# Kernel optimization log

Hardware: AMD Instinct MI355X
Metric: run time of the kernel (lower is better)

Reference implementation:

```python
import jax, jax.numpy as jnp
from jax import lax
import numpy as np

B, H, W = 16, 512, 512
NBINS = 256
MARGIN_EYE = 12
BLUR_SIZE = 5
ALPHA_SKIN, ALPHA_EYE, ALPHA_LIP = 0.3, 0.8, 0.1


def de_norm(x):
    return jnp.clip((x + 1.0) * 0.5, 0.0, 1.0)


def renorm(x):
    return x * 2.0 - 1.0


def _match_channel(src, ref, w_s, w_r):
    # src/ref: (P,) pixel values in [0,255]; w_s/w_r: (P,) mask weights
    b_s = jnp.clip(src.astype(jnp.int32), 0, NBINS - 1)
    b_r = jnp.clip(ref.astype(jnp.int32), 0, NBINS - 1)
    h_s = jnp.zeros((NBINS,), src.dtype).at[b_s].add(w_s)   # masked histogram
    h_r = jnp.zeros((NBINS,), ref.dtype).at[b_r].add(w_r)
    cdf_s = jnp.cumsum(h_s) / jnp.maximum(jnp.sum(h_s), 1e-6)
    cdf_r = jnp.cumsum(h_r) / jnp.maximum(jnp.sum(h_r), 1e-6)
    # CDF-matching transfer table (equiv. of cal_trans in PSGAN/EleGANt)
    table = jnp.clip(jnp.searchsorted(cdf_r, cdf_s), 0, NBINS - 1).astype(src.dtype)
    return table[b_s]


def masked_his_match(image_s, image_r, mask_s, mask_r):
    # image: (3,H,W), mask: (1,H,W)
    s = de_norm(image_s) * 255.0 * mask_s
    r = de_norm(image_r) * 255.0 * mask_r
    w_s = mask_s.reshape(-1)
    w_r = mask_r.reshape(-1)
    matched = jax.vmap(_match_channel, in_axes=(0, 0, None, None))(
        s.reshape(3, -1), r.reshape(3, -1), w_s, w_r).reshape(s.shape)
    matched = jnp.where(mask_s > 0, matched, s)  # only masked pixels replaced
    return renorm(matched / 255.0)


def expand_area(mask, margin):
    # morphological dilation (max pool) of (1,H,W) mask
    k = 2 * margin + 1
    return lax.reduce_window(mask, 0.0, lax.max, (1, k, k), (1, 1, 1), 'SAME')


def mask_blur(mask, blur_size):
    # box blur; 'valid' mode: blurred support kept inside original mask
    k = blur_size
    s = lax.reduce_window(mask, 0.0, lax.add, (1, k, k), (1, 1, 1), 'SAME') / float(k * k)
    return s * mask


def generate_pgt(image_s, image_r, mask_s, mask_r, lms_s, lms_r):
    pgt = image_s
    # skin (channel 1)
    m = mask_s[1:2]
    pgt = (1.0 - m) * pgt + m * masked_his_match(image_s, image_r, m, mask_r[1:2])
    # neck (channel 4)
    m = mask_s[4:5]
    pgt = (1.0 - m) * pgt + m * masked_his_match(image_s, image_r, m, mask_r[4:5])
    # lip (channel 0)
    m = mask_s[0:1]
    pgt = (1.0 - m) * pgt + m * masked_his_match(image_s, image_r, m, mask_r[0:1])
    # eyes (channels 2,3), dilated and intersected with skin
    m_se = expand_area(jnp.sum(mask_s[2:4], axis=0, keepdims=True), MARGIN_EYE) * mask_s[1:2]
    m_re = expand_area(jnp.sum(mask_r[2:4], axis=0, keepdims=True), MARGIN_EYE) * mask_r[1:2]
    eye_match = masked_his_match(image_s, image_r, m_se, m_re)
    mb = mask_blur(m_se, BLUR_SIZE)
    pgt = (1.0 - mb) * pgt + mb * eye_match
    # fine_align (reconstructed, simplified: per-region alpha blend of reference,
    # landmark warp omitted -- helper source not provided)
    for m, a in ((mask_s[1:2], ALPHA_SKIN), (m_se, ALPHA_EYE), (mask_s[0:1], ALPHA_LIP)):
        pgt = (1.0 - a * m) * pgt + (a * m) * image_r
    return pgt


def setup_inputs() -> dict:
    key = jax.random.key(0)
    ks = jax.random.split(key, 6)
    sources = jax.random.uniform(ks[0], (B, 3, H, W), jnp.float32, -1.0, 1.0)
    targets = jax.random.uniform(ks[1], (B, 3, H, W), jnp.float32, -1.0, 1.0)
    mask_srcs = (jax.random.uniform(ks[2], (B, 5, H, W)) < 0.3).astype(jnp.float32)
    mask_tars = (jax.random.uniform(ks[3], (B, 5, H, W)) < 0.3).astype(jnp.float32)
    lms_srcs = jax.random.uniform(ks[4], (B, 68, 2), jnp.float32, 0.0, float(H))
    lms_tars = jax.random.uniform(ks[5], (B, 68, 2), jnp.float32, 0.0, float(H))
    return {"sources": sources, "targets": targets, "mask_srcs": mask_srcs,
            "mask_tars": mask_tars, "lms_srcs": lms_srcs, "lms_tars": lms_tars}


def reference(sources, targets, mask_srcs, mask_tars, lms_srcs, lms_tars):
    # vmap over batch replaces the per-sample Python loop of ComposePGT.forward
    return jax.vmap(generate_pgt)(sources, targets, mask_srcs, mask_tars, lms_srcs, lms_tars)
```

## Files before the change

kernel.cpp:

```cpp
#include <hip/hip_runtime.h>
#include <stdint.h>

#define BB 16
#define HH 512
#define WW 512
#define HW (HH*WW)
#define NB 256


__device__ __forceinline__ float denorm255(float x) {
    return fminf(fmaxf((x + 1.0f) * 0.5f, 0.0f), 1.0f) * 255.0f;
}
__device__ __forceinline__ float renorm_lut(int t) {
    return ((float)t / 255.0f) * 2.0f - 1.0f;
}
__device__ __forceinline__ uint32_t alignb(uint32_t hi, uint32_t lo, int r) {
    return (uint32_t)(((((uint64_t)hi) << 32) | lo) >> (8 * r));
}

__global__ void __launch_bounds__(256) prep_hor_kernel(
    const float* __restrict__ ms, const float* __restrict__ mr,
    uint32_t* __restrict__ C, uint32_t* __restrict__ eh)
{
    int blk  = blockIdx.x;
    int side = blk >> 10;
    int rem  = blk & 1023;
    int b    = rem >> 6;
    int rg   = rem & 63;
    int r    = threadIdx.x >> 5;
    int c    = threadIdx.x & 31;
    int y    = (rg << 3) + r;

    const float* base = (side ? mr : ms) + (size_t)b * 5 * HW + (size_t)y * WW;

    float4 v[5][4];
    #pragma unroll
    for (int p = 0; p < 5; p++) {
        const float4* pp = (const float4*)(base + (size_t)p * HW);
        #pragma unroll
        for (int q = 0; q < 4; q++) v[p][q] = pp[c + 32 * q];
    }

    __shared__ uint32_t sE[8][128];
    size_t plane = (size_t)(side * BB + b);
    uint32_t* Crow = C + plane * (HW / 4) + y * 128;
    #pragma unroll
    for (int q = 0; q < 4; q++) {
        uint32_t wc = 0;
        #pragma unroll
        for (int j = 0; j < 4; j++) {
            float a0 = (&v[0][q].x)[j];
            float a1 = (&v[1][q].x)[j];
            float a2 = (&v[2][q].x)[j];
            float a3 = (&v[3][q].x)[j];
            float a4 = (&v[4][q].x)[j];
            uint32_t e  = (uint32_t)(a2 + a3);
            uint32_t pb = (a0 > 0.f ? 4u : 0u) | (a1 > 0.f ? 8u : 0u)
                        | (a4 > 0.f ? 16u : 0u);
            wc |= (e | pb) << (8 * j);
        }
        Crow[c + 32 * q] = wc;
        sE[r][c + 32 * q] = wc & 0x03030303u;
    }
    __syncthreads();

    uint32_t* Erow = eh + plane * (HW / 4) + y * 128;
    #pragma unroll
    for (int q = 0; q < 4; q++) {
        int w = c + 32 * q;
        uint32_t arr[7];
        #pragma unroll
        for (int i = 0; i < 7; i++) {
            int idx = w - 3 + i;
            arr[i] = (idx >= 0 && idx < 128) ? sE[r][idx] : 0u;
        }
        uint32_t acc = arr[3];
        #pragma unroll
        for (int s = 1; s <= 12; s++) {
            int a = s >> 2, rr = s & 3;
            uint32_t vp, vm;
            if (rr == 0) {
                vp = arr[3 + a];
                vm = arr[3 - a];
            } else {
                vp = alignb(arr[3 + a + 1], arr[3 + a], rr);
                int am = (s + 3) >> 2;
                vm = alignb(arr[3 - am + 1], arr[3 - am], 4 - rr);
            }
            acc |= vp | vm;
        }
        Erow[w] = acc;
    }
}

__global__ void __launch_bounds__(256) ver_kernel(
    const uint32_t* __restrict__ eh, uint32_t* __restrict__ C)
{
    int t   = blockIdx.x * 256 + threadIdx.x;
    int sb  = t >> 12;
    int rem = t & 4095;
    int yg  = rem >> 5;
    int ck  = rem & 31;
    int y0  = yg << 2;
    const uint4* P = (const uint4*)(eh + (size_t)sb * (HW / 4));
    auto R = [&](int y) -> uint4 {
        uint4 z = {0, 0, 0, 0};
        if (y < 0 || y >= HH) return z;
        return P[y * 32 + ck];
    };
    uint4 core = {0, 0, 0, 0};
    #pragma unroll
    for (int yy = -9; yy <= 12; yy++) {
        uint4 r = R(y0 + yy);
        core.x |= r.x; core.y |= r.y; core.z |= r.z; core.w |= r.w;
    }
    uint4 b0 = R(y0 - 12), b1 = R(y0 - 11), b2 = R(y0 - 10);
    uint4 a0 = R(y0 + 13), a1 = R(y0 + 14), a2 = R(y0 + 15);

    uint4* C4 = (uint4*)(C + (size_t)sb * (HW / 4));
    #pragma unroll
    for (int i = 0; i < 4; i++) {
        uint4 v = core;
        if (i == 0) { v.x|=b0.x|b1.x|b2.x; v.y|=b0.y|b1.y|b2.y; v.z|=b0.z|b1.z|b2.z; v.w|=b0.w|b1.w|b2.w; }
        if (i == 1) { v.x|=b1.x|b2.x|a0.x; v.y|=b1.y|b2.y|a0.y; v.z|=b1.z|b2.z|a0.z; v.w|=b1.w|b2.w|a0.w; }
        if (i == 2) { v.x|=b2.x|a0.x|a1.x; v.y|=b2.y|a0.y|a1.y; v.z|=b2.z|a0.z|a1.z; v.w|=b2.w|a0.w|a1.w; }
        if (i == 3) { v.x|=a0.x|a1.x|a2.x; v.y|=a0.y|a1.y|a2.y; v.z|=a0.z|a1.z|a2.z; v.w|=a0.w|a1.w|a2.w; }
        int idx = (y0 + i) * 32 + ck;
        uint4 cw = C4[idx];
        #pragma unroll
        for (int q = 0; q < 4; q++) {
            uint32_t vv = (&v.x)[q];
            uint32_t cc = (&cw.x)[q];
            uint32_t t3 = vv & (vv >> 1) & 0x01010101u;
            vv -= t3;
            uint32_t m1b = (cc >> 3) & 0x01010101u;
            vv &= m1b * 255u;
            (&cw.x)[q] = cc | (vv << 5);
        }
        C4[idx] = cw;
    }
}

__global__ void __launch_bounds__(256) blur_kernel(
    const uint32_t* __restrict__ C, uint4* __restrict__ mbs)
{
    int t = blockIdx.x * 256 + threadIdx.x;
    int b = t >> 14;
    int rem = t & 16383;
    int y = rem >> 5;
    int c = rem & 31;
    const uint32_t* P = C + (size_t)b * (HW / 4);
    int c4 = c << 2;
    uint32_t s[6] = {0u, 0u, 0u, 0u, 0u, 0u};
    #pragma unroll
    for (int dy = -2; dy <= 2; dy++) {
        int yy = y + dy;
        if (yy < 0 || yy >= HH) continue;
        const uint32_t* rp = P + yy * 128;
        uint32_t l = (c > 0)  ? rp[c4 - 1] : 0u;
        uint4 m = *((const uint4*)(rp + c4));
        uint32_t rr = (c < 31) ? rp[c4 + 4] : 0u;
        s[0] += (l   >> 5) & 0x03030303u;
        s[1] += (m.x >> 5) & 0x03030303u;
        s[2] += (m.y >> 5) & 0x03030303u;
        s[3] += (m.z >> 5) & 0x03030303u;
        s[4] += (m.w >> 5) & 0x03030303u;
        s[5] += (rr  >> 5) & 0x03030303u;
    }
    uint4 o;
    #pragma unroll
    for (int k = 0; k < 4; k++) {
        uint32_t v = s[k + 1];
        v += alignb(s[k + 1], s[k],     2);
        v += alignb(s[k + 1], s[k],     3);
        v += alignb(s[k + 2], s[k + 1], 1);
        v += alignb(s[k + 2], s[k + 1], 2);
        (&o.x)[k] = v;
    }
    mbs[t] = o;
}

#define HB 32
__device__ __forceinline__ void hist4(int* h, uint32_t cw,
                                      float4 v0, float4 v1, float4 v2)
{
    float d0[4] = {denorm255(v0.x), denorm255(v0.y), denorm255(v0.z), denorm255(v0.w)};
    float d1[4] = {denorm255(v1.x), denorm255(v1.y), denorm255(v1.z), denorm255(v1.w)};
    float d2[4] = {denorm255(v2.x), denorm255(v2.y), denorm255(v2.z), denorm255(v2.w)};
    #pragma unroll
    for (int j = 0; j < 4; j++) {
        uint32_t pb = (cw >> (8 * j)) & 0xFFu;
        if (pb & 8u) {
            atomicAdd(&h[0 * NB + min((int)d0[j], 255)], 1);
            atomicAdd(&h[1 * NB + min((int)d1[j], 255)], 1);
            atomicAdd(&h[2 * NB + min((int)d2[j], 255)], 1);
        }
        if (pb & 16u) {
            atomicAdd(&h[3 * NB + min((int)d0[j], 255)], 1);
            atomicAdd(&h[4 * NB + min((int)d1[j], 255)], 1);
            atomicAdd(&h[5 * NB + min((int)d2[j], 255)], 1);
        }
        if (pb & 4u) {
            atomicAdd(&h[6 * NB + min((int)d0[j], 255)], 1);
            atomicAdd(&h[7 * NB + min((int)d1[j], 255)], 1);
            atomicAdd(&h[8 * NB + min((int)d2[j], 255)], 1);
        }
        int mei = (int)((pb >> 5) & 3u);
        if (mei) {
            float fm = (float)mei;
            atomicAdd(&h[ 9 * NB + min((int)(d0[j] * fm), 255)], mei);
            atomicAdd(&h[10 * NB + min((int)(d1[j] * fm), 255)], mei);
            atomicAdd(&h[11 * NB + min((int)(d2[j] * fm), 255)], mei);
        }
    }
}

__global__ void __launch_bounds__(256) hist_kernel(
    const float* __restrict__ src, const float* __restrict__ tgt,
    const uint32_t* __restrict__ C, int* __restrict__ hist)
{
    int bs  = blockIdx.x / HB;
    int blk = blockIdx.x % HB;
    int b = bs >> 1, side = bs & 1;
    const float* img = (side ? tgt : src) + (size_t)b * 3 * HW;
    const float4* i0 = (const float4*)(img);
    const float4* i1 = (const float4*)(img + HW);
    const float4* i2 = (const float4*)(img + 2 * (size_t)HW);
    const uint2* pc = (const uint2*)(C + (size_t)(side * BB + b) * (HW / 4));

    __shared__ int h[2][12 * NB];
    int* hw = h[threadIdx.x >> 7];
    for (int i = threadIdx.x; i < 2 * 12 * NB; i += 256) ((int*)h)[i] = 0;
    __syncthreads();

    for (int c = blk * 256 + threadIdx.x; c < HW / 8; c += HB * 256) {
        uint2 cw = pc[c];
        float4 a0 = i0[2 * c], b0 = i0[2 * c + 1];
        float4 a1 = i1[2 * c], b1 = i1[2 * c + 1];
        float4 a2 = i2[2 * c], b2 = i2[2 * c + 1];
        hist4(hw, cw.x, a0, a1, a2);
        hist4(hw, cw.y, b0, b1, b2);
    }
    __syncthreads();
    int* gh = hist + (size_t)bs * 12 * NB;
    for (int i = threadIdx.x; i < 12 * NB; i += 256) {
        int s = h[0][i] + h[1][i];
        if (s) atomicAdd(&gh[i], s);
    }
}

__global__ void __launch_bounds__(NB) table_kernel(
    const int* __restrict__ hist, uint8_t* __restrict__ table)
{
    int idx = blockIdx.x;
    int c = idx % 3; int rest = idx / 3; int rg = rest & 3; int b = rest >> 2;
    const int* hs = hist + ((size_t)((b * 2 + 0) * 4 + rg) * 3 + c) * NB;
    const int* hr = hist + ((size_t)((b * 2 + 1) * 4 + rg) * 3 + c) * NB;
    __shared__ int a[NB];
    __shared__ float cr[NB];
    int t = threadIdx.x;

    a[t] = hs[t];
    __syncthreads();
    for (int off = 1; off < NB; off <<= 1) {
        int v = (t >= off) ? a[t - off] : 0;
        __syncthreads();
        a[t] += v;
        __syncthreads();
    }
    int totS = a[NB - 1];
    int cumS = a[t];
    __syncthreads();

    a[t] = hr[t];
    __syncthreads();
    for (int off = 1; off < NB; off <<= 1) {
        int v = (t >= off) ? a[t - off] : 0;
        __syncthreads();
        a[t] += v;
        __syncthreads();
    }
    int totR = a[NB - 1];
    cr[t] = (float)a[t] / fmaxf((float)totR, 1e-6f);
    float v = (float)cumS / fmaxf((float)totS, 1e-6f);
    __syncthreads();

    int cnt = 0;
    for (int j = 0; j < NB; j++) cnt += (cr[j] < v) ? 1 : 0;
    table[(size_t)idx * NB + t] = (uint8_t)min(cnt, 255);
}

__device__ __forceinline__ void proc4(uint32_t cw, uint32_t qw,
    float4 x0, float4 x1, float4 x2, float4 r0, float4 r1, float4 r2,
    const uint8_t* tb, float4& o0, float4& o1, float4& o2)
{
    float X0[4] = {x0.x, x0.y, x0.z, x0.w};
    float X1[4] = {x1.x, x1.y, x1.z, x1.w};
    float X2[4] = {x2.x, x2.y, x2.z, x2.w};
    float R0[4] = {r0.x, r0.y, r0.z, r0.w};
    float R1[4] = {r1.x, r1.y, r1.z, r1.w};
    float R2[4] = {r2.x, r2.y, r2.z, r2.w};
    #pragma unroll
    for (int j = 0; j < 4; j++) {
        uint32_t pb = (cw >> (8 * j)) & 0xFFu;
        float q = (float)((qw >> (8 * j)) & 0xFFu);
        float m0f = (float)((pb >> 2) & 1u);
        float m1f = (float)((pb >> 3) & 1u);
        float m4f = (float)((pb >> 4) & 1u);
        float fm  = (float)((pb >> 5) & 3u);
        float d0 = denorm255(X0[j]), d1 = denorm255(X1[j]), d2 = denorm255(X2[j]);
        float p0 = X0[j], p1 = X1[j], p2 = X2[j];
        {
            float e0 = renorm_lut(tb[0 * NB + min((int)(d0 * m1f), 255)]);
            float e1 = renorm_lut(tb[1 * NB + min((int)(d1 * m1f), 255)]);
            float e2 = renorm_lut(tb[2 * NB + min((int)(d2 * m1f), 255)]);
            p0 = (1.0f - m1f) * p0 + m1f * e0;
            p1 = (1.0f - m1f) * p1 + m1f * e1;
            p2 = (1.0f - m1f) * p2 + m1f * e2;
        }
        {
            float e0 = renorm_lut(tb[3 * NB + min((int)(d0 * m4f), 255)]);
            float e1 = renorm_lut(tb[4 * NB + min((int)(d1 * m4f), 255)]);
            float e2 = renorm_lut(tb[5 * NB + min((int)(d2 * m4f), 255)]);
            p0 = (1.0f - m4f) * p0 + m4f * e0;
            p1 = (1.0f - m4f) * p1 + m4f * e1;
            p2 = (1.0f - m4f) * p2 + m4f * e2;
        }
        {
            float e0 = renorm_lut(tb[6 * NB + min((int)(d0 * m0f), 255)]);
            float e1 = renorm_lut(tb[7 * NB + min((int)(d1 * m0f), 255)]);
            float e2 = renorm_lut(tb[8 * NB + min((int)(d2 * m0f), 255)]);
            p0 = (1.0f - m0f) * p0 + m0f * e0;
            p1 = (1.0f - m0f) * p1 + m0f * e1;
            p2 = (1.0f - m0f) * p2 + m0f * e2;
        }
        {
            float mb = (q * (1.0f / 25.0f)) * fm;
            float e0 = renorm_lut(tb[ 9 * NB + min((int)(d0 * fm), 255)]);
            float e1 = renorm_lut(tb[10 * NB + min((int)(d1 * fm), 255)]);
            float e2 = renorm_lut(tb[11 * NB + min((int)(d2 * fm), 255)]);
            p0 = (1.0f - mb) * p0 + mb * e0;
            p1 = (1.0f - mb) * p1 + mb * e1;
            p2 = (1.0f - mb) * p2 + mb * e2;
        }
        float a = 0.3f * m1f;
        p0 = (1.0f - a) * p0 + a * R0[j];
        p1 = (1.0f - a) * p1 + a * R1[j];
        p2 = (1.0f - a) * p2 + a * R2[j];
        a = 0.8f * fm;
        p0 = (1.0f - a) * p0 + a * R0[j];
        p1 = (1.0f - a) * p1 + a * R1[j];
        p2 = (1.0f - a) * p2 + a * R2[j];
        a = 0.1f * m0f;
        p0 = (1.0f - a) * p0 + a * R0[j];
        p1 = (1.0f - a) * p1 + a * R1[j];
        p2 = (1.0f - a) * p2 + a * R2[j];
        (&o0.x)[j] = p0; (&o1.x)[j] = p1; (&o2.x)[j] = p2;
    }
}

__global__ void __launch_bounds__(256) compose_kernel(
    const float* __restrict__ src, const float* __restrict__ tgt,
    const uint32_t* __restrict__ C, const uint32_t* __restrict__ mbs,
    const uint8_t* __restrict__ table, float* __restrict__ out)
{
    int t = blockIdx.x * 256 + threadIdx.x;
    int b = t >> 15;
    int c = t & 32767;

    __shared__ uint8_t tb[12 * NB];
    {
        const uint32_t* gt = (const uint32_t*)(table + (size_t)b * 12 * NB);
        uint32_t* tw = (uint32_t*)tb;
        for (int i = threadIdx.x; i < 12 * NB / 4; i += 256) tw[i] = gt[i];
    }
    __syncthreads();

    const float4* s0 = (const float4*)(src + (size_t)b * 3 * HW);
    const float4* s1 = s0 + HW / 4;
    const float4* s2 = s1 + HW / 4;
    const float4* t0 = (const float4*)(tgt + (size_t)b * 3 * HW);
    const float4* t1 = t0 + HW / 4;
    const float4* t2 = t1 + HW / 4;
    const uint2* pc = (const uint2*)(C + (size_t)b * (HW / 4));
    const uint2* qc = (const uint2*)(mbs + (size_t)b * (HW / 4));
    float4* o0 = (float4*)(out + (size_t)b * 3 * HW);
    float4* o1 = o0 + HW / 4;
    float4* o2 = o1 + HW / 4;

    uint2 cw = pc[c];
    uint2 qw = qc[c];
    float4 xa0 = s0[2 * c], xb0 = s0[2 * c + 1];
    float4 xa1 = s1[2 * c], xb1 = s1[2 * c + 1];
    float4 xa2 = s2[2 * c], xb2 = s2[2 * c + 1];
    float4 ra0 = t0[2 * c], rb0 = t0[2 * c + 1];
    float4 ra1 = t1[2 * c], rb1 = t1[2 * c + 1];
    float4 ra2 = t2[2 * c], rb2 = t2[2 * c + 1];

    float4 oa0, oa1, oa2, ob0, ob1, ob2;
    proc4(cw.x, qw.x, xa0, xa1, xa2, ra0, ra1, ra2, tb, oa0, oa1, oa2);
    proc4(cw.y, qw.y, xb0, xb1, xb2, rb0, rb1, rb2, tb, ob0, ob1, ob2);

    o0[2 * c] = oa0; o0[2 * c + 1] = ob0;
    o1[2 * c] = oa1; o1[2 * c + 1] = ob1;
    o2[2 * c] = oa2; o2[2 * c + 1] = ob2;
}

extern "C" void kernel_launch(void* const* d_in, const int* in_sizes, int n_in,
                              void* d_out, int out_size, void* d_ws, size_t ws_size,
                              hipStream_t stream) {
    const float* src = (const float*)d_in[0];
    const float* tgt = (const float*)d_in[1];
    const float* ms  = (const float*)d_in[2];
    const float* mr  = (const float*)d_in[3];
    float* out = (float*)d_out;

    uint8_t* ws = (uint8_t*)d_ws;
    uint32_t* C   = (uint32_t*)(ws);
    uint32_t* eh  = (uint32_t*)(ws + (size_t)2 * BB * HW);
    uint32_t* mbs = (uint32_t*)(ws + (size_t)4 * BB * HW);
    int* hist     = (int*)(ws + (size_t)5 * BB * HW);
    uint8_t* table = ws + (size_t)5 * BB * HW + (size_t)2 * BB * 12 * NB * 4;

    hipMemsetAsync(hist, 0, (size_t)2 * BB * 12 * NB * sizeof(int), stream);

    prep_hor_kernel<<<2 * BB * 64, 256, 0, stream>>>(ms, mr, C, eh);
    ver_kernel<<<2 * BB * (HH / 4) * (WW / 16) / 256, 256, 0, stream>>>(eh, C);
    blur_kernel<<<BB * (HW / 16) / 256, 256, 0, stream>>>(C, (uint4*)mbs);
    hist_kernel<<<2 * BB * HB, 256, 0, stream>>>(src, tgt, C, hist);
    table_kernel<<<BB * 4 * 3, NB, 0, stream>>>(hist, table);
    compose_kernel<<<BB * (HW / 8) / 256, 256, 0, stream>>>(src, tgt, C, mbs, table, out);
}
```

Measured before the change: 328.3 us.

## Give each thread contiguous words and use wave shuffles instead of shared-memory halo

Result: no change. 330.7 us (+0.7%).

```diff
diff --git a/kernel.cpp b/kernel.cpp
--- a/kernel.cpp
+++ b/kernel.cpp
@@ -18,7 +18,7 @@
     return (uint32_t)(((((uint64_t)hi) << 32) | lo) >> (8 * r));
 }
 
-__global__ void __launch_bounds__(256) prep_hor_kernel(
+__global__ void __launch_bounds__(256, 4) prep_hor_kernel(
     const float* __restrict__ ms, const float* __restrict__ mr,
     uint32_t* __restrict__ C, uint32_t* __restrict__ eh)
 {
@@ -38,59 +38,67 @@
     for (int p = 0; p < 5; p++) {
         const float4* pp = (const float4*)(base + (size_t)p * HW);
         #pragma unroll
-        for (int q = 0; q < 4; q++) v[p][q] = pp[c + 32 * q];
-    }
-
-    __shared__ uint32_t sE[8][128];
-    size_t plane = (size_t)(side * BB + b);
-    uint32_t* Crow = C + plane * (HW / 4) + y * 128;
-    #pragma unroll
-    for (int q = 0; q < 4; q++) {
+        for (int j = 0; j < 4; j++) v[p][j] = pp[4 * c + j];
+    }
+
+    uint32_t Wd[4], E[4];
+    #pragma unroll
+    for (int j = 0; j < 4; j++) {
         uint32_t wc = 0;
         #pragma unroll
-        for (int j = 0; j < 4; j++) {
-            float a0 = (&v[0][q].x)[j];
-            float a1 = (&v[1][q].x)[j];
-            float a2 = (&v[2][q].x)[j];
-            float a3 = (&v[3][q].x)[j];
-            float a4 = (&v[4][q].x)[j];
+        for (int k = 0; k < 4; k++) {
+            float a0 = (&v[0][j].x)[k];
+            float a1 = (&v[1][j].x)[k];
+            float a2 = (&v[2][j].x)[k];
+            float a3 = (&v[3][j].x)[k];
+            float a4 = (&v[4][j].x)[k];
             uint32_t e  = (uint32_t)(a2 + a3);
             uint32_t pb = (a0 > 0.f ? 4u : 0u) | (a1 > 0.f ? 8u : 0u)
                         | (a4 > 0.f ? 16u : 0u);
-            wc |= (e | pb) << (8 * j);
-        }
-        Crow[c + 32 * q] = wc;
-        sE[r][c + 32 * q] = wc & 0x03030303u;
-    }
-    __syncthreads();
-
-    uint32_t* Erow = eh + plane * (HW / 4) + y * 128;
-    #pragma unroll
-    for (int q = 0; q < 4; q++) {
-        int w = c + 32 * q;
-        uint32_t arr[7];
-        #pragma unroll
-        for (int i = 0; i < 7; i++) {
-            int idx = w - 3 + i;
-            arr[i] = (idx >= 0 && idx < 128) ? sE[r][idx] : 0u;
-        }
-        uint32_t acc = arr[3];
+            wc |= (e | pb) << (8 * k);
+        }
+        Wd[j] = wc;
+        E[j]  = wc & 0x03030303u;
+    }
+
+    size_t plane = (size_t)(side * BB + b);
+    uint32_t* Crow = C + plane * (HW / 4) + y * 128;
+    *((uint4*)(Crow + 4 * c)) = make_uint4(Wd[0], Wd[1], Wd[2], Wd[3]);
+
+    uint32_t Lw[3], Rw[3];
+    #pragma unroll
+    for (int i = 0; i < 3; i++) {
+        uint32_t lv = __shfl_up(E[i + 1], 1, 32);
+        Lw[i] = (c == 0) ? 0u : lv;
+        uint32_t rv = __shfl_down(E[i], 1, 32);
+        Rw[i] = (c == 31) ? 0u : rv;
+    }
+    uint32_t arr[10] = {Lw[0], Lw[1], Lw[2], E[0], E[1], E[2], E[3],
+                        Rw[0], Rw[1], Rw[2]};
+
+    uint32_t acc[4];
+    #pragma unroll
+    for (int k = 0; k < 4; k++) {
+        const int b3 = 3 + k;
+        uint32_t a = arr[b3];
         #pragma unroll
         for (int s = 1; s <= 12; s++) {
-            int a = s >> 2, rr = s & 3;
+            int ai = s >> 2, rr = s & 3;
             uint32_t vp, vm;
             if (rr == 0) {
-                vp = arr[3 + a];
-                vm = arr[3 - a];
+                vp = arr[b3 + ai];
+                vm = arr[b3 - ai];
             } else {
-                vp = alignb(arr[3 + a + 1], arr[3 + a], rr);
+                vp = alignb(arr[b3 + ai + 1], arr[b3 + ai], rr);
                 int am = (s + 3) >> 2;
-                vm = alignb(arr[3 - am + 1], arr[3 - am], 4 - rr);
+                vm = alignb(arr[b3 - am + 1], arr[b3 - am], 4 - rr);
             }
-            acc |= vp | vm;
-        }
-        Erow[w] = acc;
-    }
+            a |= vp | vm;
+        }
+        acc[k] = a;
+    }
+    uint32_t* Erow = eh + plane * (HW / 4) + y * 128;
+    *((uint4*)(Erow + 4 * c)) = make_uint4(acc[0], acc[1], acc[2], acc[3]);
 }
 
 __global__ void __launch_bounds__(256) ver_kernel(
```
